# Kernel optimization log

Hardware: AMD Instinct MI355X
Metric: run time of the kernel (lower is better)

The kernel has to match this reference:

```python
import jax, jax.numpy as jnp
import numpy as np

M, K, N = 8192, 4096, 4096  # tokens, in_features, out_features


def setup_inputs() -> dict:
    key = jax.random.key(0)
    k1, k2, k3, k4, k5, k6 = jax.random.split(key, 6)
    return {
        "x_q": jax.random.randint(k1, (M, K), 0, 256, dtype=jnp.int32),
        "weight_int8": jax.random.randint(k2, (N, K), 0, 256, dtype=jnp.int32),
        "weight_scale": jax.random.uniform(k3, (N, 1), dtype=jnp.float32) * 0.01 + 1e-4,
        "weight_zero_point": jax.random.randint(k4, (N, 1), 0, 256, dtype=jnp.int32),
        "bias": jax.random.normal(k5, (N,), dtype=jnp.float32),
        "input_scale": jax.random.uniform(k6, (1,), dtype=jnp.float32) * 0.05 + 1e-4,
        "input_zero_point": 128,
    }


def reference(x_q, weight_int8, weight_scale, weight_zero_point, bias, input_scale, input_zero_point):
    # zero-point-subtracted fp32 operands (simulated int32 accumulation in fp32)
    x_f = x_q.astype(jnp.float32) - jnp.float32(input_zero_point)      # [M, K]
    w_f = weight_int8.astype(jnp.float32) - weight_zero_point.astype(jnp.float32)  # [N, K]
    acc = jnp.einsum('mk,nk->mn', x_f, w_f)                            # [M, N]
    dequant_scale = input_scale * weight_scale.T                       # [1, N]
    return acc * dequant_scale + bias                                  # [M, N]
```

## Files before the change

### kernel.cpp

```cpp
#include <hip/hip_runtime.h>
#include <hip/hip_bf16.h>
#include <stdint.h>

typedef int v4i __attribute__((ext_vector_type(4)));

#define AS_GLOBAL(p) ((const __attribute__((address_space(1))) void*)(p))
#define AS_LDS(p)    ((__attribute__((address_space(3))) void*)(p))

__global__ __launch_bounds__(256) void prep_x_kernel(const int* __restrict__ x,
                                                     const int* __restrict__ izp_p,
                                                     signed char* __restrict__ xs,
                                                     int* __restrict__ rowsum, int K) {
    int row = blockIdx.x;
    int izp = izp_p[0];
    const int4* xr = (const int4*)(x + (long)row * K);
    uint32_t* xo = (uint32_t*)(xs + (long)row * K);
    int sum = 0;
    int n4 = K >> 2;
    for (int i = threadIdx.x; i < n4; i += 256) {
        int4 v = xr[i];
        int a0 = v.x - izp, a1 = v.y - izp, a2 = v.z - izp, a3 = v.w - izp;
        sum += a0 + a1 + a2 + a3;
        xo[i] = (uint32_t)(a0 & 0xFF) | ((uint32_t)(a1 & 0xFF) << 8) |
                ((uint32_t)(a2 & 0xFF) << 16) | ((uint32_t)(a3 & 0xFF) << 24);
    }
    sum += __shfl_down(sum, 32);
    sum += __shfl_down(sum, 16);
    sum += __shfl_down(sum, 8);
    sum += __shfl_down(sum, 4);
    sum += __shfl_down(sum, 2);
    sum += __shfl_down(sum, 1);
    __shared__ int red[4];
    if ((threadIdx.x & 63) == 0) red[threadIdx.x >> 6] = sum;
    __syncthreads();
    if (threadIdx.x == 0) rowsum[row] = red[0] + red[1] + red[2] + red[3];
}

__global__ __launch_bounds__(256) void prep_w_kernel(const int* __restrict__ w,
                                                     signed char* __restrict__ ws, int K) {
    int row = blockIdx.x;
    const int4* wr = (const int4*)(w + (long)row * K);
    uint32_t* wo = (uint32_t*)(ws + (long)row * K);
    int n4 = K >> 2;
    for (int i = threadIdx.x; i < n4; i += 256) {
        int4 v = wr[i];
        int a0 = v.x - 128, a1 = v.y - 128, a2 = v.z - 128, a3 = v.w - 128;
        wo[i] = (uint32_t)(a0 & 0xFF) | ((uint32_t)(a1 & 0xFF) << 8) |
                ((uint32_t)(a2 & 0xFF) << 16) | ((uint32_t)(a3 & 0xFF) << 24);
    }
}


#define BAR  __builtin_amdgcn_s_barrier()
#define PHASE_END do { asm volatile("s_waitcnt lgkmcnt(0)" ::: "memory"); \
                       __builtin_amdgcn_sched_barrier(0); BAR; } while (0)
#define VM4  asm volatile("s_waitcnt vmcnt(4)" ::: "memory")
#define PRIO1 __builtin_amdgcn_s_setprio(1)
#define PRIO0 __builtin_amdgcn_s_setprio(0)

#define STAGE(gbase, opofs, half, buf, tile) do {                                     \
    int t_ = (tile); if (t_ >= NT) t_ -= NT;                                          \
    const signed char* src_ = (gbase) + (long)((half) * 128) * K + (long)t_ * 128;    \
    signed char* dst_ = ldsw + (buf) * 65536 + (opofs) + (half) * 16384;              \
    __builtin_amdgcn_global_load_lds(AS_GLOBAL(src_), AS_LDS(dst_), 16, 0, 0);        \
    __builtin_amdgcn_global_load_lds(AS_GLOBAL(src_ + 64L * K), AS_LDS(dst_ + 8192), 16, 0, 0); \
  } while (0)

#define READ_A(buf, mi) do {                                                          \
    af[mi][0] = *(const v4i*)(lds + (buf) * 65536 + aoff0 + (mi) * 2048);             \
    af[mi][1] = *(const v4i*)(lds + (buf) * 65536 + aoff1 + (mi) * 2048); } while (0)
#define READ_B(buf, ni) do {                                                          \
    bf[ni][0] = *(const v4i*)(lds + (buf) * 65536 + boff0 + (ni) * 2048);             \
    bf[ni][1] = *(const v4i*)(lds + (buf) * 65536 + boff1 + (ni) * 2048); } while (0)

#define MFMA_1(mi, ni, ks)                                                             \
    acc[mi][ni] = __builtin_amdgcn_mfma_i32_16x16x64_i8(af[mi][ks], bf[ni][ks], acc[mi][ni], 0, 0, 0);

#define MFMAQ(mb, nb) do {                                                             \
    MFMA_1(mb + 0, nb + 0, 0) MFMA_1(mb + 0, nb + 1, 0)                                \
    MFMA_1(mb + 1, nb + 0, 0) MFMA_1(mb + 1, nb + 1, 0)                                \
    MFMA_1(mb + 2, nb + 0, 0) MFMA_1(mb + 2, nb + 1, 0)                                \
    MFMA_1(mb + 3, nb + 0, 0) MFMA_1(mb + 3, nb + 1, 0)                                \
    MFMA_1(mb + 0, nb + 0, 1) MFMA_1(mb + 0, nb + 1, 1)                                \
    MFMA_1(mb + 1, nb + 0, 1) MFMA_1(mb + 1, nb + 1, 1)                                \
    MFMA_1(mb + 2, nb + 0, 1) MFMA_1(mb + 2, nb + 1, 1)                                \
    MFMA_1(mb + 3, nb + 0, 1) MFMA_1(mb + 3, nb + 1, 1) } while (0)

#define KTILE(b, tA, tB) do {                                                          \
                                                                    \
    READ_A(b, 0); READ_A(b, 1); READ_B(b, 0); READ_B(b, 1);                            \
    READ_A(b, 2); READ_A(b, 3);                                                        \
    STAGE(gA, 0, 0, (b) ^ 1, tA);                                                      \
    BAR;                                                                               \
    PRIO1; MFMAQ(0, 0); PRIO0;                                                         \
    PHASE_END;                                                                         \
                                                                     \
    READ_B(b, 2); READ_B(b, 3);                                                        \
    STAGE(gA, 0, 1, (b) ^ 1, tA);                                                      \
    BAR;                                                                               \
    PRIO1; MFMAQ(0, 2); PRIO0;                                                         \
    PHASE_END;                                                                         \
                                                                     \
    READ_A(b, 4); READ_A(b, 5); READ_A(b, 6); READ_A(b, 7);                            \
    STAGE(gB, 32768, 0, (b), tB);                                                      \
    BAR;                                                                               \
    PRIO1; MFMAQ(4, 0); PRIO0;                                                         \
    PHASE_END;                                                                         \
                                                                    \
    STAGE(gB, 32768, 1, (b), tB);                                                      \
    BAR;                                                                               \
    PRIO1; MFMAQ(4, 2); PRIO0; VM4;                                                    \
    PHASE_END;                                                                         \
  } while (0)

__global__ __launch_bounds__(512, 2) void gemm_i8_8ph(
    const signed char* __restrict__ A,
    const signed char* __restrict__ B,
    const int* __restrict__ rowsum, const float* __restrict__ wscale,
    const int* __restrict__ wzp, const float* __restrict__ bias,
    const float* __restrict__ iscale, float* __restrict__ C,
    int M, int N, int K) {
  __shared__ signed char lds[131072];
  const int tid = threadIdx.x;
  const int w = tid >> 6, l = tid & 63;
  const int wm = w >> 2, wn = w & 3;
  const int fr = l & 15, fq = l >> 4;

  int nwg = gridDim.x, bid = blockIdx.x;
  if ((nwg & 7) == 0) { int cpx = nwg >> 3; bid = (bid & 7) * cpx + (bid >> 3); }
  const int ntiles = N >> 8;
  const int mt = bid / ntiles, nt = bid - mt * ntiles;
  const long brow = (long)mt << 8, bcol = (long)nt << 8;

  const int NT = K >> 7;
  const int NI = NT >> 1;

  const int srow = w * 8 + (l >> 3);
  const int schunk = ((l & 7) ^ (l >> 3)) << 4;
  const signed char* gA = A + (brow + srow) * (long)K + schunk;
  const signed char* gB = B + (bcol + srow) * (long)K + schunk;
  signed char* ldsw = lds + w * 1024;

  const int axor = fr & 7;
  const int aoff0 = (wm * 128 + fr) * 128 + ((fq ^ axor) << 4);
  const int aoff1 = (wm * 128 + fr) * 128 + (((4 + fq) ^ axor) << 4);
  const int boff0 = 32768 + (wn * 64 + fr) * 128 + ((fq ^ axor) << 4);
  const int boff1 = 32768 + (wn * 64 + fr) * 128 + (((4 + fq) ^ axor) << 4);

  v4i acc[8][4] = {};
  v4i af[8][2], bf[4][2];

  STAGE(gB, 32768, 0, 0, 0); STAGE(gB, 32768, 1, 0, 0);
  STAGE(gA, 0, 0, 0, 0);     STAGE(gA, 0, 1, 0, 0);
  STAGE(gB, 32768, 0, 1, 1); STAGE(gB, 32768, 1, 1, 1);
  VM4; BAR;

  for (int i = 0; i < NI; ++i) {
    const int t1 = 2 * i + 1, t2 = 2 * i + 2, t3 = 2 * i + 3;
    KTILE(0, t1, t2);
    KTILE(1, t2, t3);
  }

  const float is = iscale[0];
  int rs[8][4];
#pragma unroll
  for (int mi = 0; mi < 8; ++mi)
#pragma unroll
    for (int j = 0; j < 4; ++j)
      rs[mi][j] = rowsum[(int)brow + wm * 128 + mi * 16 + fq * 4 + j];
#pragma unroll
  for (int ni = 0; ni < 4; ++ni) {
    const int col = (int)bcol + wn * 64 + ni * 16 + fr;
    const float sc = is * wscale[col];
    const int zpc = 128 - wzp[col];
    const float bi = bias[col];
#pragma unroll
    for (int mi = 0; mi < 8; ++mi) {
      const int row0 = (int)brow + wm * 128 + mi * 16 + fq * 4;
#pragma unroll
      for (int j = 0; j < 4; ++j) {
        const int v = acc[mi][ni][j] + zpc * rs[mi][j];
        C[(long)(row0 + j) * N + col] = (float)v * sc + bi;
      }
    }
  }
}

extern "C" void kernel_launch(void* const* d_in, const int* in_sizes, int n_in,
                              void* d_out, int out_size, void* d_ws, size_t ws_size,
                              hipStream_t stream) {
    const int* x_q = (const int*)d_in[0];
    const int* w_q = (const int*)d_in[1];
    const float* wscale = (const float*)d_in[2];
    const int* wzp = (const int*)d_in[3];
    const float* bias = (const float*)d_in[4];
    const float* iscale = (const float*)d_in[5];
    const int* izp = (const int*)d_in[6];

    int N = in_sizes[2];
    int K = in_sizes[1] / N;
    int M = in_sizes[0] / K;

    signed char* xs = (signed char*)d_ws;
    signed char* wsq = xs + (size_t)M * K;
    int* rowsum = (int*)(wsq + (size_t)N * K);

    prep_x_kernel<<<M, 256, 0, stream>>>(x_q, izp, xs, rowsum, K);
    prep_w_kernel<<<N, 256, 0, stream>>>(w_q, wsq, K);

    int grid = (M / 256) * (N / 256);
    gemm_i8_8ph<<<grid, 512, 0, stream>>>(xs, wsq, rowsum, wscale, wzp, bias, iscale,
                                          (float*)d_out, M, N, K);
}
```

Before: 193.1 us.

## Switch int8 GEMM from 16x16x64 to 32x32x32 MFMA tiles

Replaces the 16x16x64 i8 MFMA instruction with 32x32x32 i8 MFMA, reorganizing per-wave fragments into 4x2 32x32 accumulator tiles with new LDS read offsets and swizzled k-chunks, and rewrites the epilogue to the 32x32 output layout. Larger MFMA tiles mean fewer LDS fragment reads per FLOP and fewer issued instructions. The MFMA phases are reordered so that K-chunks are split across phases instead of M/N blocks. Risks include different register pressure and LDS bank-conflict patterns with the new lane-to-row mapping.

```diff
diff --git a/kernel.cpp b/kernel.cpp
--- a/kernel.cpp
+++ b/kernel.cpp
@@ -2,7 +2,8 @@
 #include <hip/hip_bf16.h>
 #include <stdint.h>
 
-typedef int v4i __attribute__((ext_vector_type(4)));
+typedef int v4i  __attribute__((ext_vector_type(4)));
+typedef int v16i __attribute__((ext_vector_type(16)));
 
 #define AS_GLOBAL(p) ((const __attribute__((address_space(1))) void*)(p))
 #define AS_LDS(p)    ((__attribute__((address_space(3))) void*)(p))
@@ -66,50 +67,44 @@
     __builtin_amdgcn_global_load_lds(AS_GLOBAL(src_ + 64L * K), AS_LDS(dst_ + 8192), 16, 0, 0); \
   } while (0)
 
-#define READ_A(buf, mi) do {                                                          \
-    af[mi][0] = *(const v4i*)(lds + (buf) * 65536 + aoff0 + (mi) * 2048);             \
-    af[mi][1] = *(const v4i*)(lds + (buf) * 65536 + aoff1 + (mi) * 2048); } while (0)
-#define READ_B(buf, ni) do {                                                          \
-    bf[ni][0] = *(const v4i*)(lds + (buf) * 65536 + boff0 + (ni) * 2048);             \
-    bf[ni][1] = *(const v4i*)(lds + (buf) * 65536 + boff1 + (ni) * 2048); } while (0)
-
-#define MFMA_1(mi, ni, ks)                                                             \
-    acc[mi][ni] = __builtin_amdgcn_mfma_i32_16x16x64_i8(af[mi][ks], bf[ni][ks], acc[mi][ni], 0, 0, 0);
-
-#define MFMAQ(mb, nb) do {                                                             \
-    MFMA_1(mb + 0, nb + 0, 0) MFMA_1(mb + 0, nb + 1, 0)                                \
-    MFMA_1(mb + 1, nb + 0, 0) MFMA_1(mb + 1, nb + 1, 0)                                \
-    MFMA_1(mb + 2, nb + 0, 0) MFMA_1(mb + 2, nb + 1, 0)                                \
-    MFMA_1(mb + 3, nb + 0, 0) MFMA_1(mb + 3, nb + 1, 0)                                \
-    MFMA_1(mb + 0, nb + 0, 1) MFMA_1(mb + 0, nb + 1, 1)                                \
-    MFMA_1(mb + 1, nb + 0, 1) MFMA_1(mb + 1, nb + 1, 1)                                \
-    MFMA_1(mb + 2, nb + 0, 1) MFMA_1(mb + 2, nb + 1, 1)                                \
-    MFMA_1(mb + 3, nb + 0, 1) MFMA_1(mb + 3, nb + 1, 1) } while (0)
+#define READ_A(buf, mi, ks)                                                           \
+    af[mi][ks] = *(const v4i*)(lds + (buf) * 65536 + abase##mi + (kc##ks << 4));
+#define READ_B(buf, ni, ks)                                                           \
+    bf[ni][ks] = *(const v4i*)(lds + (buf) * 65536 + bbase##ni + (kc##ks << 4));
+
+#define MM(mi, ni, ks)                                                                 \
+    acc[(mi)*2+(ni)] = __builtin_amdgcn_mfma_i32_32x32x32_i8(af[mi][ks], bf[ni][ks],  \
+                                                             acc[(mi)*2+(ni)], 0, 0, 0);
+#define MFMA8(m0, m1, k0, k1) do {                                                     \
+    MM(m0, 0, k0) MM(m0, 1, k0) MM(m1, 0, k0) MM(m1, 1, k0)                            \
+    MM(m0, 0, k1) MM(m0, 1, k1) MM(m1, 0, k1) MM(m1, 1, k1) } while (0)
 
 #define KTILE(b, tA, tB) do {                                                          \
-                                                                    \
-    READ_A(b, 0); READ_A(b, 1); READ_B(b, 0); READ_B(b, 1);                            \
-    READ_A(b, 2); READ_A(b, 3);                                                        \
+                                                                              \
+    READ_A(b, 0, 0) READ_A(b, 1, 0) READ_B(b, 0, 0) READ_B(b, 1, 0)                    \
+    READ_A(b, 0, 1) READ_A(b, 1, 1) READ_B(b, 0, 1) READ_B(b, 1, 1)                    \
     STAGE(gA, 0, 0, (b) ^ 1, tA);                                                      \
     BAR;                                                                               \
-    PRIO1; MFMAQ(0, 0); PRIO0;                                                         \
-    PHASE_END;                                                                         \
-                                                                     \
-    READ_B(b, 2); READ_B(b, 3);                                                        \
+    PRIO1; MFMA8(0, 1, 0, 1); PRIO0;                                                   \
+    PHASE_END;                                                                         \
+                                                                              \
+    READ_A(b, 0, 2) READ_A(b, 1, 2) READ_B(b, 0, 2) READ_B(b, 1, 2)                    \
+    READ_A(b, 0, 3) READ_A(b, 1, 3) READ_B(b, 0, 3) READ_B(b, 1, 3)                    \
     STAGE(gA, 0, 1, (b) ^ 1, tA);                                                      \
     BAR;                                                                               \
-    PRIO1; MFMAQ(0, 2); PRIO0;                                                         \
-    PHASE_END;                                                                         \
-                                                                     \
-    READ_A(b, 4); READ_A(b, 5); READ_A(b, 6); READ_A(b, 7);                            \
+    PRIO1; MFMA8(0, 1, 2, 3); PRIO0;                                                   \
+    PHASE_END;                                                                         \
+                                                                              \
+    READ_A(b, 2, 0) READ_A(b, 3, 0) READ_A(b, 2, 1) READ_A(b, 3, 1)                    \
     STAGE(gB, 32768, 0, (b), tB);                                                      \
     BAR;                                                                               \
-    PRIO1; MFMAQ(4, 0); PRIO0;                                                         \
-    PHASE_END;                                                                         \
-                                                                    \
+    PRIO1; MFMA8(2, 3, 0, 1); PRIO0;                                                   \
+    PHASE_END;                                                                         \
+                                                                              \
+    READ_A(b, 2, 2) READ_A(b, 3, 2) READ_A(b, 2, 3) READ_A(b, 3, 3)                    \
     STAGE(gB, 32768, 1, (b), tB);                                                      \
     BAR;                                                                               \
-    PRIO1; MFMAQ(4, 2); PRIO0; VM4;                                                    \
+    PRIO1; MFMA8(2, 3, 2, 3); PRIO0; VM4;                                              \
     PHASE_END;                                                                         \
   } while (0)
 
@@ -124,7 +119,6 @@
   const int tid = threadIdx.x;
   const int w = tid >> 6, l = tid & 63;
   const int wm = w >> 2, wn = w & 3;
-  const int fr = l & 15, fq = l >> 4;
 
   int nwg = gridDim.x, bid = blockIdx.x;
   if ((nwg & 7) == 0) { int cpx = nwg >> 3; bid = (bid & 7) * cpx + (bid >> 3); }
@@ -141,14 +135,20 @@
   const signed char* gB = B + (bcol + srow) * (long)K + schunk;
   signed char* ldsw = lds + w * 1024;
 
-  const int axor = fr & 7;
-  const int aoff0 = (wm * 128 + fr) * 128 + ((fq ^ axor) << 4);
-  const int aoff1 = (wm * 128 + fr) * 128 + (((4 + fq) ^ axor) << 4);
-  const int boff0 = 32768 + (wn * 64 + fr) * 128 + ((fq ^ axor) << 4);
-  const int boff1 = 32768 + (wn * 64 + fr) * 128 + (((4 + fq) ^ axor) << 4);
-
-  v4i acc[8][4] = {};
-  v4i af[8][2], bf[4][2];
+  const int lr = l & 31, hi = l >> 5, xr = l & 7;
+  const int abase0 = (wm * 128 + 0  * 32 + lr) * 128;
+  const int abase1 = (wm * 128 + 1  * 32 + lr) * 128;
+  const int abase2 = (wm * 128 + 2  * 32 + lr) * 128;
+  const int abase3 = (wm * 128 + 3  * 32 + lr) * 128;
+  const int bbase0 = 32768 + (wn * 64 + 0 * 32 + lr) * 128;
+  const int bbase1 = 32768 + (wn * 64 + 1 * 32 + lr) * 128;
+  const int kc0 = (0 * 2 + hi) ^ xr;
+  const int kc1 = (1 * 2 + hi) ^ xr;
+  const int kc2 = (2 * 2 + hi) ^ xr;
+  const int kc3 = (3 * 2 + hi) ^ xr;
+
+  v16i acc[8] = {};
+  v4i af[4][4], bf[2][4];
 
   STAGE(gB, 32768, 0, 0, 0); STAGE(gB, 32768, 1, 0, 0);
   STAGE(gA, 0, 0, 0, 0);     STAGE(gA, 0, 1, 0, 0);
@@ -162,25 +162,25 @@
   }
 
   const float is = iscale[0];
-  int rs[8][4];
-#pragma unroll
-  for (int mi = 0; mi < 8; ++mi)
-#pragma unroll
-    for (int j = 0; j < 4; ++j)
-      rs[mi][j] = rowsum[(int)brow + wm * 128 + mi * 16 + fq * 4 + j];
-#pragma unroll
-  for (int ni = 0; ni < 4; ++ni) {
-    const int col = (int)bcol + wn * 64 + ni * 16 + fr;
+  int rs[4][16];
+#pragma unroll
+  for (int mi = 0; mi < 4; ++mi)
+#pragma unroll
+    for (int reg = 0; reg < 16; ++reg)
+      rs[mi][reg] = rowsum[(int)brow + wm * 128 + mi * 32 + (reg & 3) + 8 * (reg >> 2) + 4 * hi];
+#pragma unroll
+  for (int ni = 0; ni < 2; ++ni) {
+    const int col = (int)bcol + wn * 64 + ni * 32 + lr;
     const float sc = is * wscale[col];
     const int zpc = 128 - wzp[col];
     const float bi = bias[col];
 #pragma unroll
-    for (int mi = 0; mi < 8; ++mi) {
-      const int row0 = (int)brow + wm * 128 + mi * 16 + fq * 4;
-#pragma unroll
-      for (int j = 0; j < 4; ++j) {
-        const int v = acc[mi][ni][j] + zpc * rs[mi][j];
-        C[(long)(row0 + j) * N + col] = (float)v * sc + bi;
+    for (int mi = 0; mi < 4; ++mi) {
+#pragma unroll
+      for (int reg = 0; reg < 16; ++reg) {
+        const int row = (int)brow + wm * 128 + mi * 32 + (reg & 3) + 8 * (reg >> 2) + 4 * hi;
+        const int v = acc[mi * 2 + ni][reg] + zpc * rs[mi][reg];
+        C[(long)row * N + col] = (float)v * sc + bi;
       }
     }
   }
```

Result: slower. 217.0 us (+12.4%).
